# Performance work log

Measured on AMD Instinct MI355X. Metric: run time of the kernel, lower is better.

The kernel has to match this reference:

```python
import jax, jax.numpy as jnp
import numpy as np


def setup_inputs() -> dict:
    key = jax.random.key(0)
    ks = jax.random.split(key, 5)
    D, H, S, B = 2048, 16, 2048, 2
    kd = D // H
    scale = 0.02
    return {
        "in_x": jax.random.normal(ks[0], (B, S, D), dtype=jnp.float32),
        "W_sc": jax.random.normal(ks[1], (D, D), dtype=jnp.float32) * scale,
        "b_sc": jax.random.normal(ks[2], (D,), dtype=jnp.float32) * scale,
        "W_qkv": jax.random.normal(ks[3], (D, D + 2 * kd), dtype=jnp.float32) * scale,
        "b_qkv": jax.random.normal(ks[4], (D + 2 * kd,), dtype=jnp.float32) * scale,
        "head_num": 16,
    }


def reference(in_x, W_sc, b_sc, W_qkv, b_qkv, head_num):
    B, S, D = in_x.shape
    kd = D // head_num
    # two independent linear projections
    short_cut = in_x @ W_sc + b_sc                      # [B,S,D]
    qkv = in_x @ W_qkv + b_qkv                          # [B,S,D+2*kd]
    q = qkv[..., :D].reshape(B, S, head_num, kd).transpose(0, 2, 1, 3)  # [B,H,S,kd]
    k = qkv[..., D:D + kd]                              # [B,S,kd] shared single K head
    v = qkv[..., D + kd:]                               # [B,S,kd] shared single V head
    # NOTE: faithful to source, scale is k_dim**2, not sqrt(k_dim)
    score = jnp.einsum("bhsd,btd->bhst", q, k) / float(kd * kd)         # [B,H,S,S]
    atten = jnp.einsum("bhst,btd->bhsd", jax.nn.softmax(score, axis=-1), v)  # [B,H,S,kd]
    res = atten.transpose(0, 2, 1, 3).reshape(B, S, D)  # [B,S,D]
    return (score, atten, res, short_cut)
```

## Files before the change

kernel.cpp:

```cpp
#include <hip/hip_runtime.h>
#include <math.h>

#define M_    4096
#define D_    2048
#define NQKV  2304
#define NFUSE 4352
#define KD_   128
#define S_    2048

using bf16x8  = __attribute__((ext_vector_type(8))) __bf16;
using f32x4   = __attribute__((ext_vector_type(4))) float;
using ushort8 = __attribute__((ext_vector_type(8))) unsigned short;

__device__ __forceinline__ unsigned short f2bf(float f) {
  unsigned int u = __builtin_bit_cast(unsigned int, f);
  u += 0x7fffu + ((u >> 16) & 1u);
  return (unsigned short)(u >> 16);
}

#define GLL16(g, l) \
  __builtin_amdgcn_global_load_lds((__attribute__((address_space(1))) void*)(g), \
                                   (__attribute__((address_space(3))) void*)(l), 16, 0, 0)

__global__ void cast_x_kernel(const float* __restrict__ x, unsigned short* __restrict__ xb) {
  int i = (blockIdx.x * 256 + threadIdx.x) * 8;
  float4 a = *(const float4*)(x + i);
  float4 b = *(const float4*)(x + i + 4);
  ushort8 o;
  o[0]=f2bf(a.x); o[1]=f2bf(a.y); o[2]=f2bf(a.z); o[3]=f2bf(a.w);
  o[4]=f2bf(b.x); o[5]=f2bf(b.y); o[6]=f2bf(b.z); o[7]=f2bf(b.w);
  *(ushort8*)(xb + i) = o;
}

__global__ void prep_w_kernel(const float* __restrict__ Wsc, const float* __restrict__ Wqkv,
                              unsigned short* __restrict__ Wt) {
  __shared__ float t[32][33];
  int k0 = blockIdx.x * 32, n0 = blockIdx.y * 32;
  int tx = threadIdx.x, ty = threadIdx.y;
  #pragma unroll
  for (int i = 0; i < 32; i += 8) {
    int k = k0 + ty + i, n = n0 + tx;
    t[ty + i][tx] = (n < D_) ? Wsc[(size_t)k * D_ + n] : Wqkv[(size_t)k * NQKV + (n - D_)];
  }
  __syncthreads();
  #pragma unroll
  for (int i = 0; i < 32; i += 8) {
    int n = n0 + ty + i, k = k0 + tx;
    Wt[(size_t)n * D_ + k] = f2bf(t[tx][ty + i]);
  }
}

__global__ __launch_bounds__(256, 2) void gemm_fused_kernel(
    const unsigned short* __restrict__ X,
    const unsigned short* __restrict__ Wt,
    const float* __restrict__ b_sc, const float* __restrict__ b_qkv,
    float* __restrict__ shortcut, unsigned short* __restrict__ qkv) {
  __shared__ alignas(16) unsigned short As[128 * 32];
  __shared__ alignas(16) unsigned short Bs[128 * 32];
  const int tid = threadIdx.x;
  const int lane = tid & 63, wid = tid >> 6;
  const int l16 = lane & 15, quad = lane >> 4;
  const int wm = (wid >> 1) * 64, wn = (wid & 1) * 64;
  const int m0 = blockIdx.y * 128, n0 = blockIdx.x * 128;

  const int fa = tid * 16;
  const char* aSrc0 = (const char*)X  + (size_t)(m0 + (fa >> 6)) * 4096 + (fa & 63);
  const char* aSrc1 = aSrc0 + (size_t)64 * 4096;
  const char* bSrc0 = (const char*)Wt + (size_t)(n0 + (fa >> 6)) * 4096 + (fa & 63);
  const char* bSrc1 = bSrc0 + (size_t)64 * 4096;
  char* aDst0 = (char*)As + fa; char* aDst1 = aDst0 + 4096;
  char* bDst0 = (char*)Bs + fa; char* bDst1 = bDst0 + 4096;

  f32x4 acc[4][4] = {};
  for (int kt = 0; kt < 64; ++kt) {
    __syncthreads();
    GLL16(aSrc0, aDst0); GLL16(aSrc1, aDst1);
    GLL16(bSrc0, bDst0); GLL16(bSrc1, bDst1);
    aSrc0 += 64; aSrc1 += 64; bSrc0 += 64; bSrc1 += 64;
    __syncthreads();
    bf16x8 af[4], bfr[4];
    #pragma unroll
    for (int mi = 0; mi < 4; ++mi)
      af[mi] = *(const bf16x8*)(As + (wm + mi * 16 + l16) * 32 + quad * 8);
    #pragma unroll
    for (int ni = 0; ni < 4; ++ni)
      bfr[ni] = *(const bf16x8*)(Bs + (wn + ni * 16 + l16) * 32 + quad * 8);
    #pragma unroll
    for (int mi = 0; mi < 4; ++mi)
      #pragma unroll
      for (int ni = 0; ni < 4; ++ni)
        acc[mi][ni] = __builtin_amdgcn_mfma_f32_16x16x32_bf16(af[mi], bfr[ni], acc[mi][ni], 0, 0, 0);
  }

  #pragma unroll
  for (int ni = 0; ni < 4; ++ni) {
    int n = n0 + wn + ni * 16 + l16;
    float bias = (n < D_) ? b_sc[n] : b_qkv[n - D_];
    #pragma unroll
    for (int mi = 0; mi < 4; ++mi) {
      #pragma unroll
      for (int r = 0; r < 4; ++r) {
        int m = m0 + wm + mi * 16 + quad * 4 + r;
        float v = acc[mi][ni][r] + bias;
        if (n < D_) shortcut[(size_t)m * D_ + n] = v;
        else        qkv[(size_t)m * NQKV + (n - D_)] = f2bf(v);
      }
    }
  }
}

__global__ void prep_vt_kernel(const unsigned short* __restrict__ qkv,
                               unsigned short* __restrict__ vt) {
  __shared__ unsigned short t[32][33];
  int b = blockIdx.z;
  int t0 = blockIdx.x * 32, d0 = blockIdx.y * 32;
  int tx = threadIdx.x, ty = threadIdx.y;
  #pragma unroll
  for (int i = 0; i < 32; i += 8)
    t[ty + i][tx] = qkv[(size_t)(b * S_ + t0 + ty + i) * NQKV + (D_ + KD_) + d0 + tx];
  __syncthreads();
  #pragma unroll
  for (int i = 0; i < 32; i += 8)
    vt[(size_t)(b * KD_ + d0 + ty + i) * S_ + t0 + tx] = t[tx][ty + i];
}

__global__ __launch_bounds__(256, 2) void attn_kernel(
    const unsigned short* __restrict__ qkv,
    const unsigned short* __restrict__ vt,
    float* __restrict__ score, float* __restrict__ atten, float* __restrict__ res) {
  __shared__ alignas(16) unsigned short Qs[4 * 64 * 32];
  __shared__ alignas(16) unsigned short Ks[4 * 64 * 32];
  __shared__ alignas(16) unsigned short Vs[2 * 128 * 32];
  __shared__ alignas(16) unsigned short Ps[2 * 64 * 32];

  const int tid = threadIdx.x;
  const int lane = tid & 63, wid = tid >> 6;
  const int l16 = lane & 15, quad = lane >> 4;
  const int qt = blockIdx.x, bh = blockIdx.y;
  const int b = bh >> 4, h = bh & 15;
  const int q0 = qt * 64;

  {
    const char* qb = (const char*)qkv + (size_t)(b * S_ + q0) * (NQKV * 2) + h * (KD_ * 2);
    #pragma unroll
    for (int i = 0; i < 4; ++i) {
      int f = tid * 16 + i * 4096;
      GLL16(qb + (size_t)((f & 4095) >> 6) * (NQKV * 2) + (f >> 12) * 64 + (f & 63),
            (char*)Qs + f);
    }
  }
  __syncthreads();
  bf16x8 qf[4];
  #pragma unroll
  for (int kk = 0; kk < 4; ++kk)
    qf[kk] = *(const bf16x8*)(Qs + kk * 2048 + (wid * 16 + l16) * 32 + quad * 8);

  f32x4 acc_o[8] = {};
  float m_r[4] = {-1e30f, -1e30f, -1e30f, -1e30f};
  float l_r[4] = {0.f, 0.f, 0.f, 0.f};
  const float inv_scale = 1.0f / 16384.0f;

  const char* kb0 = (const char*)qkv + (size_t)b * S_ * (NQKV * 2) + D_ * 2;
  const char* vb0 = (const char*)vt + (size_t)b * KD_ * S_ * 2;

  for (int tt = 0; tt < 32; ++tt) {
    const int t0 = tt * 64;
    __syncthreads();
    #pragma unroll
    for (int i = 0; i < 4; ++i) {
      int f = tid * 16 + i * 4096;
      GLL16(kb0 + (size_t)(t0 + ((f & 4095) >> 6)) * (NQKV * 2) + (f >> 12) * 64 + (f & 63),
            (char*)Ks + f);
    }
    #pragma unroll
    for (int i = 0; i < 4; ++i) {
      int f = tid * 16 + i * 4096;
      GLL16(vb0 + (size_t)((f & 8191) >> 6) * (S_ * 2) + t0 * 2 + (f >> 13) * 64 + (f & 63),
            (char*)Vs + f);
    }
    __syncthreads();

    f32x4 sa[4];
    #pragma unroll
    for (int jn = 0; jn < 4; ++jn) {
      f32x4 a = {};
      #pragma unroll
      for (int kk = 0; kk < 4; ++kk) {
        bf16x8 kf = *(const bf16x8*)(Ks + kk * 2048 + (jn * 16 + l16) * 32 + quad * 8);
        a = __builtin_amdgcn_mfma_f32_16x16x32_bf16(qf[kk], kf, a, 0, 0, 0);
      }
      #pragma unroll
      for (int r = 0; r < 4; ++r) a[r] *= inv_scale;
      sa[jn] = a;
    }

    {
      float* sc = score + ((size_t)bh * S_ + q0 + wid * 16) * S_ + t0;
      #pragma unroll
      for (int jn = 0; jn < 4; ++jn)
        #pragma unroll
        for (int r = 0; r < 4; ++r)
          sc[(size_t)(quad * 4 + r) * S_ + jn * 16 + l16] = sa[jn][r];
    }

    float mx[4];
    #pragma unroll
    for (int r = 0; r < 4; ++r)
      mx[r] = fmaxf(fmaxf(sa[0][r], sa[1][r]), fmaxf(sa[2][r], sa[3][r]));
    #pragma unroll
    for (int off = 8; off >= 1; off >>= 1)
      #pragma unroll
      for (int r = 0; r < 4; ++r) mx[r] = fmaxf(mx[r], __shfl_xor(mx[r], off, 16));
    float alpha[4];
    #pragma unroll
    for (int r = 0; r < 4; ++r) {
      float mn = fmaxf(m_r[r], mx[r]);
      alpha[r] = __expf(m_r[r] - mn);
      m_r[r] = mn;
    }
    float sm[4] = {0.f, 0.f, 0.f, 0.f};
    #pragma unroll
    for (int jn = 0; jn < 4; ++jn)
      #pragma unroll
      for (int r = 0; r < 4; ++r) {
        float p = __expf(sa[jn][r] - m_r[r]);
        sa[jn][r] = p;
        sm[r] += p;
      }
    #pragma unroll
    for (int off = 8; off >= 1; off >>= 1)
      #pragma unroll
      for (int r = 0; r < 4; ++r) sm[r] += __shfl_xor(sm[r], off, 16);
    #pragma unroll
    for (int r = 0; r < 4; ++r) l_r[r] = l_r[r] * alpha[r] + sm[r];
    #pragma unroll
    for (int dn = 0; dn < 8; ++dn)
      #pragma unroll
      for (int r = 0; r < 4; ++r) acc_o[dn][r] *= alpha[r];

    #pragma unroll
    for (int jn = 0; jn < 4; ++jn) {
      int t = jn * 16 + l16;
      #pragma unroll
      for (int r = 0; r < 4; ++r)
        Ps[(t >> 5) * 2048 + (wid * 16 + quad * 4 + r) * 32 + (t & 31)] = f2bf(sa[jn][r]);
    }
    __syncthreads();

    #pragma unroll
    for (int kkt = 0; kkt < 2; ++kkt) {
      bf16x8 pf = *(const bf16x8*)(Ps + kkt * 2048 + (wid * 16 + l16) * 32 + quad * 8);
      #pragma unroll
      for (int dn = 0; dn < 8; ++dn) {
        bf16x8 vf = *(const bf16x8*)(Vs + kkt * 4096 + (dn * 16 + l16) * 32 + quad * 8);
        acc_o[dn] = __builtin_amdgcn_mfma_f32_16x16x32_bf16(pf, vf, acc_o[dn], 0, 0, 0);
      }
    }
  }

  #pragma unroll
  for (int dn = 0; dn < 8; ++dn) {
    int d = dn * 16 + l16;
    #pragma unroll
    for (int r = 0; r < 4; ++r) {
      int q = q0 + wid * 16 + quad * 4 + r;
      float v = acc_o[dn][r] / l_r[r];
      atten[((size_t)bh * S_ + q) * KD_ + d] = v;
      res[((size_t)b * S_ + q) * D_ + h * KD_ + d] = v;
    }
  }
}

extern "C" void kernel_launch(void* const* d_in, const int* in_sizes, int n_in,
                              void* d_out, int out_size, void* d_ws, size_t ws_size,
                              hipStream_t stream) {
  (void)in_sizes; (void)n_in; (void)out_size; (void)ws_size;
  const float* in_x  = (const float*)d_in[0];
  const float* W_sc  = (const float*)d_in[1];
  const float* b_sc  = (const float*)d_in[2];
  const float* W_qkv = (const float*)d_in[3];
  const float* b_qkv = (const float*)d_in[4];

  char* ws = (char*)d_ws;
  unsigned short* Xb  = (unsigned short*)ws;
  unsigned short* Wt  = (unsigned short*)(ws + 16777216);
  unsigned short* qkv = (unsigned short*)(ws + 16777216 + 17825792);
  unsigned short* Vt  = (unsigned short*)(ws + 16777216 + 17825792 + 18874368);

  float* score    = (float*)d_out;
  float* atten    = score + 134217728;
  float* res      = atten + 8388608;
  float* shortcut = res + 8388608;

  cast_x_kernel<<<4096, 256, 0, stream>>>(in_x, Xb);
  prep_w_kernel<<<dim3(64, 136), dim3(32, 8), 0, stream>>>(W_sc, W_qkv, Wt);
  gemm_fused_kernel<<<dim3(34, 32), 256, 0, stream>>>(Xb, Wt, b_sc, b_qkv, shortcut, qkv);
  prep_vt_kernel<<<dim3(64, 4, 2), dim3(32, 8), 0, stream>>>(qkv, Vt);
  attn_kernel<<<dim3(32, 32), 256, 0, stream>>>(qkv, Vt, score, atten, res);
}
```

Before: 910.8 us.

## Transpose score MFMA, widen key tiles, vectorize score stores, remap blocks per XCD

The attention kernel now computes S^T by swapping the MFMA operands, so each lane holds four consecutive key columns of one query row. This lets score writes become 16-byte vector stores and reduces the softmax to a single row value per lane. The key tile grows from 64 to 128, which halves the loop iterations and barriers at the cost of more LDS. Q is loaded straight into registers, and both the GEMM and attention grids are flattened with an XCD-aware block remap to improve L2 locality.

```diff
diff --git a/kernel.cpp b/kernel.cpp
--- a/kernel.cpp
+++ b/kernel.cpp
@@ -4,7 +4,6 @@
 #define M_    4096
 #define D_    2048
 #define NQKV  2304
-#define NFUSE 4352
 #define KD_   128
 #define S_    2048
 
@@ -16,6 +15,9 @@
   unsigned int u = __builtin_bit_cast(unsigned int, f);
   u += 0x7fffu + ((u >> 16) & 1u);
   return (unsigned short)(u >> 16);
+}
+__device__ __forceinline__ unsigned int pack2bf(float a, float b) {
+  return (unsigned int)f2bf(a) | ((unsigned int)f2bf(b) << 16);
 }
 
 #define GLL16(g, l) \
@@ -61,7 +63,9 @@
   const int lane = tid & 63, wid = tid >> 6;
   const int l16 = lane & 15, quad = lane >> 4;
   const int wm = (wid >> 1) * 64, wn = (wid & 1) * 64;
-  const int m0 = blockIdx.y * 128, n0 = blockIdx.x * 128;
+  const int bid = blockIdx.x;
+  const int wg = (bid & 7) * 136 + (bid >> 3);
+  const int m0 = (wg / 34) * 128, n0 = (wg % 34) * 128;
 
   const int fa = tid * 16;
   const char* aSrc0 = (const char*)X  + (size_t)(m0 + (fa >> 6)) * 4096 + (fa & 63);
@@ -128,127 +132,106 @@
     const unsigned short* __restrict__ qkv,
     const unsigned short* __restrict__ vt,
     float* __restrict__ score, float* __restrict__ atten, float* __restrict__ res) {
-  __shared__ alignas(16) unsigned short Qs[4 * 64 * 32];
-  __shared__ alignas(16) unsigned short Ks[4 * 64 * 32];
-  __shared__ alignas(16) unsigned short Vs[2 * 128 * 32];
-  __shared__ alignas(16) unsigned short Ps[2 * 64 * 32];
+  __shared__ alignas(16) unsigned short Ks[4 * 128 * 32];
+  __shared__ alignas(16) unsigned short Vs[4 * 128 * 32];
+  __shared__ alignas(16) unsigned short Ps[4 * 64 * 32];
 
   const int tid = threadIdx.x;
   const int lane = tid & 63, wid = tid >> 6;
   const int l16 = lane & 15, quad = lane >> 4;
-  const int qt = blockIdx.x, bh = blockIdx.y;
+  const int bid = blockIdx.x;
+  const int wg = (bid & 7) * 128 + (bid >> 3);
+  const int qt = wg & 31, bh = wg >> 5;
   const int b = bh >> 4, h = bh & 15;
   const int q0 = qt * 64;
-
+  const int rr = tid >> 2, cc = (tid & 3) * 16;
+
+  bf16x8 qf[4];
   {
-    const char* qb = (const char*)qkv + (size_t)(b * S_ + q0) * (NQKV * 2) + h * (KD_ * 2);
-    #pragma unroll
-    for (int i = 0; i < 4; ++i) {
-      int f = tid * 16 + i * 4096;
-      GLL16(qb + (size_t)((f & 4095) >> 6) * (NQKV * 2) + (f >> 12) * 64 + (f & 63),
-            (char*)Qs + f);
-    }
-  }
-  __syncthreads();
-  bf16x8 qf[4];
-  #pragma unroll
-  for (int kk = 0; kk < 4; ++kk)
-    qf[kk] = *(const bf16x8*)(Qs + kk * 2048 + (wid * 16 + l16) * 32 + quad * 8);
+    const unsigned short* qb = qkv + (size_t)(b * S_ + q0 + wid * 16 + l16) * NQKV + h * KD_ + quad * 8;
+    #pragma unroll
+    for (int kk = 0; kk < 4; ++kk) qf[kk] = *(const bf16x8*)(qb + kk * 32);
+  }
 
   f32x4 acc_o[8] = {};
-  float m_r[4] = {-1e30f, -1e30f, -1e30f, -1e30f};
-  float l_r[4] = {0.f, 0.f, 0.f, 0.f};
+  float m_r = -1e30f, l_r = 0.f;
   const float inv_scale = 1.0f / 16384.0f;
 
   const char* kb0 = (const char*)qkv + (size_t)b * S_ * (NQKV * 2) + D_ * 2;
   const char* vb0 = (const char*)vt + (size_t)b * KD_ * S_ * 2;
 
-  for (int tt = 0; tt < 32; ++tt) {
-    const int t0 = tt * 64;
-    __syncthreads();
-    #pragma unroll
-    for (int i = 0; i < 4; ++i) {
-      int f = tid * 16 + i * 4096;
-      GLL16(kb0 + (size_t)(t0 + ((f & 4095) >> 6)) * (NQKV * 2) + (f >> 12) * 64 + (f & 63),
-            (char*)Ks + f);
-    }
-    #pragma unroll
-    for (int i = 0; i < 4; ++i) {
-      int f = tid * 16 + i * 4096;
-      GLL16(vb0 + (size_t)((f & 8191) >> 6) * (S_ * 2) + t0 * 2 + (f >> 13) * 64 + (f & 63),
-            (char*)Vs + f);
-    }
-    __syncthreads();
-
-    f32x4 sa[4];
-    #pragma unroll
-    for (int jn = 0; jn < 4; ++jn) {
+  for (int tt = 0; tt < 16; ++tt) {
+    const int t0 = tt * 128;
+    __syncthreads();
+    #pragma unroll
+    for (int i = 0; i < 8; ++i) {
+      int kk = i >> 1, t = (i & 1) * 64 + rr;
+      GLL16(kb0 + (size_t)(t0 + t) * (NQKV * 2) + kk * 64 + cc, (char*)Ks + i * 4096 + tid * 16);
+    }
+    #pragma unroll
+    for (int i = 0; i < 8; ++i) {
+      int kkt = i >> 1, d = (i & 1) * 64 + rr;
+      GLL16(vb0 + (size_t)d * (S_ * 2) + t0 * 2 + kkt * 64 + cc, (char*)Vs + i * 4096 + tid * 16);
+    }
+    __syncthreads();
+
+    f32x4 sa[8], sb[8];
+    #pragma unroll
+    for (int jt = 0; jt < 8; ++jt) {
       f32x4 a = {};
       #pragma unroll
       for (int kk = 0; kk < 4; ++kk) {
-        bf16x8 kf = *(const bf16x8*)(Ks + kk * 2048 + (jn * 16 + l16) * 32 + quad * 8);
-        a = __builtin_amdgcn_mfma_f32_16x16x32_bf16(qf[kk], kf, a, 0, 0, 0);
+        bf16x8 kf = *(const bf16x8*)(Ks + kk * 4096 + (jt * 16 + l16) * 32 + quad * 8);
+        a = __builtin_amdgcn_mfma_f32_16x16x32_bf16(kf, qf[kk], a, 0, 0, 0);
       }
       #pragma unroll
       for (int r = 0; r < 4; ++r) a[r] *= inv_scale;
-      sa[jn] = a;
-    }
+      sa[jt] = a; sb[jt] = a;
+    }
+
+    float mx = sa[0][0];
+    #pragma unroll
+    for (int jt = 0; jt < 8; ++jt)
+      #pragma unroll
+      for (int r = 0; r < 4; ++r) mx = fmaxf(mx, sa[jt][r]);
+    mx = fmaxf(mx, __shfl_xor(mx, 16));
+    mx = fmaxf(mx, __shfl_xor(mx, 32));
+    float mn = fmaxf(m_r, mx);
+    float alpha = __expf(m_r - mn);
+    m_r = mn;
+    float sm = 0.f;
+    #pragma unroll
+    for (int jt = 0; jt < 8; ++jt)
+      #pragma unroll
+      for (int r = 0; r < 4; ++r) { float p = __expf(sa[jt][r] - mn); sa[jt][r] = p; sm += p; }
+    sm += __shfl_xor(sm, 16);
+    sm += __shfl_xor(sm, 32);
+    l_r = l_r * alpha + sm;
+    float al[4];
+    #pragma unroll
+    for (int r = 0; r < 4; ++r) al[r] = __shfl(alpha, quad * 4 + r);
+    #pragma unroll
+    for (int dn = 0; dn < 8; ++dn)
+      #pragma unroll
+      for (int r = 0; r < 4; ++r) acc_o[dn][r] *= al[r];
 
     {
-      float* sc = score + ((size_t)bh * S_ + q0 + wid * 16) * S_ + t0;
-      #pragma unroll
-      for (int jn = 0; jn < 4; ++jn)
-        #pragma unroll
-        for (int r = 0; r < 4; ++r)
-          sc[(size_t)(quad * 4 + r) * S_ + jn * 16 + l16] = sa[jn][r];
-    }
-
-    float mx[4];
-    #pragma unroll
-    for (int r = 0; r < 4; ++r)
-      mx[r] = fmaxf(fmaxf(sa[0][r], sa[1][r]), fmaxf(sa[2][r], sa[3][r]));
-    #pragma unroll
-    for (int off = 8; off >= 1; off >>= 1)
-      #pragma unroll
-      for (int r = 0; r < 4; ++r) mx[r] = fmaxf(mx[r], __shfl_xor(mx[r], off, 16));
-    float alpha[4];
-    #pragma unroll
-    for (int r = 0; r < 4; ++r) {
-      float mn = fmaxf(m_r[r], mx[r]);
-      alpha[r] = __expf(m_r[r] - mn);
-      m_r[r] = mn;
-    }
-    float sm[4] = {0.f, 0.f, 0.f, 0.f};
-    #pragma unroll
-    for (int jn = 0; jn < 4; ++jn)
-      #pragma unroll
-      for (int r = 0; r < 4; ++r) {
-        float p = __expf(sa[jn][r] - m_r[r]);
-        sa[jn][r] = p;
-        sm[r] += p;
-      }
-    #pragma unroll
-    for (int off = 8; off >= 1; off >>= 1)
-      #pragma unroll
-      for (int r = 0; r < 4; ++r) sm[r] += __shfl_xor(sm[r], off, 16);
-    #pragma unroll
-    for (int r = 0; r < 4; ++r) l_r[r] = l_r[r] * alpha[r] + sm[r];
-    #pragma unroll
-    for (int dn = 0; dn < 8; ++dn)
-      #pragma unroll
-      for (int r = 0; r < 4; ++r) acc_o[dn][r] *= alpha[r];
-
-    #pragma unroll
-    for (int jn = 0; jn < 4; ++jn) {
-      int t = jn * 16 + l16;
-      #pragma unroll
-      for (int r = 0; r < 4; ++r)
-        Ps[(t >> 5) * 2048 + (wid * 16 + quad * 4 + r) * 32 + (t & 31)] = f2bf(sa[jn][r]);
-    }
-    __syncthreads();
-
-    #pragma unroll
-    for (int kkt = 0; kkt < 2; ++kkt) {
+      const int qrow = wid * 16 + l16;
+      #pragma unroll
+      for (int jt = 0; jt < 8; ++jt) {
+        uint2 w; w.x = pack2bf(sa[jt][0], sa[jt][1]); w.y = pack2bf(sa[jt][2], sa[jt][3]);
+        *(uint2*)(Ps + (jt >> 1) * 2048 + qrow * 32 + (jt & 1) * 16 + quad * 4) = w;
+      }
+    }
+
+    {
+      float* sc = score + ((size_t)bh * S_ + q0 + wid * 16 + l16) * S_ + t0 + quad * 4;
+      #pragma unroll
+      for (int jt = 0; jt < 8; ++jt) *(f32x4*)(sc + jt * 16) = sb[jt];
+    }
+
+    #pragma unroll
+    for (int kkt = 0; kkt < 4; ++kkt) {
       bf16x8 pf = *(const bf16x8*)(Ps + kkt * 2048 + (wid * 16 + l16) * 32 + quad * 8);
       #pragma unroll
       for (int dn = 0; dn < 8; ++dn) {
@@ -258,13 +241,16 @@
     }
   }
 
+  float lo[4];
+  #pragma unroll
+  for (int r = 0; r < 4; ++r) lo[r] = 1.0f / __shfl(l_r, quad * 4 + r);
   #pragma unroll
   for (int dn = 0; dn < 8; ++dn) {
     int d = dn * 16 + l16;
     #pragma unroll
     for (int r = 0; r < 4; ++r) {
       int q = q0 + wid * 16 + quad * 4 + r;
-      float v = acc_o[dn][r] / l_r[r];
+      float v = acc_o[dn][r] * lo[r];
       atten[((size_t)bh * S_ + q) * KD_ + d] = v;
       res[((size_t)b * S_ + q) * D_ + h * KD_ + d] = v;
     }
@@ -294,7 +280,7 @@
 
   cast_x_kernel<<<4096, 256, 0, stream>>>(in_x, Xb);
   prep_w_kernel<<<dim3(64, 136), dim3(32, 8), 0, stream>>>(W_sc, W_qkv, Wt);
-  gemm_fused_kernel<<<dim3(34, 32), 256, 0, stream>>>(Xb, Wt, b_sc, b_qkv, shortcut, qkv);
+  gemm_fused_kernel<<<1088, 256, 0, stream>>>(Xb, Wt, b_sc, b_qkv, shortcut, qkv);
   prep_vt_kernel<<<dim3(64, 4, 2), dim3(32, 8), 0, stream>>>(qkv, Vt);
-  attn_kernel<<<dim3(32, 32), 256, 0, stream>>>(qkv, Vt, score, atten, res);
-}
+  attn_kernel<<<1024, 256, 0, stream>>>(qkv, Vt, score, atten, res);
+}
```

Result: no change. 908.9 us (-0.2%).
